# Optimization experiments

Hardware: AMD Instinct MI355X
Metric: run time of the kernel (lower is better)

Reference implementation:

```python
import jax, jax.numpy as jnp
import numpy as np
from jax.scipy.special import logsumexp

AND_SCALE = 1.0e5      # Minish scale used in And
EV_SCALE = 1.0e9       # Maxish scale / large_number used in Eventually
MASK_VALUE = -1.0e9    # -large_number fill for masked entries


def maxish(x, scale, axis):
    # stljax Maxish with scale > 0: logsumexp(scale*x)/scale (stable)
    return logsumexp(x * scale, axis=axis) / scale


def minish(x, scale, axis):
    return -maxish(-x, scale, axis)


def eventually_trace(s):
    # s: [B, T] robustness trace; interval = [0, T], padding='last'
    B, T = s.shape
    rows = jnp.arange(2 * T + 1)[:, None]   # padded time index i
    cols = jnp.arange(T)[None, :]           # output time index j
    # subsignal_mask (tril): j <= i ; time_interval_mask: (i - j <= T) & (j <= i)
    mask = (cols <= rows) & (rows - cols <= T)          # [2T+1, T]
    padded = jnp.concatenate(
        [s, jnp.broadcast_to(s[:, -1:], (B, T + 1))], axis=1
    )  # [B, 2T+1], padding='last'
    mat = jnp.where(mask[None, :, :], padded[:, :, None], MASK_VALUE)  # [B, 2T+1, T]
    return maxish(mat, EV_SCALE, axis=1)  # [B, T]


def channel_trace(c):
    # And(GreaterThan(c, 0), LessThan(c, 0)) -> Minish over stacked (c, -c)
    anded = minish(jnp.stack([c, -c], axis=-1), AND_SCALE, -1)  # [B, T]
    return eventually_trace(anded)


def setup_inputs() -> dict:
    key = jax.random.key(0)
    signal = jax.random.normal(key, (32, 1024, 2), dtype=jnp.float32)
    return {"signal": signal}


def reference(signal):
    x = signal[:, :, 0]
    y = signal[:, :, 1]
    final = channel_trace(x)
    final_2 = channel_trace(y)
    return (final, final_2)
```

## Files before the change

kernel.cpp:

```cpp
#include <hip/hip_runtime.h>
#include <cfloat>
#include <cmath>


__global__ __launch_bounds__(1024) void stl_suffix_kernel(
    const float* __restrict__ sig,
    float* __restrict__ out,
    int B, int T)
{
    const int b = blockIdx.x;
    const int t = threadIdx.x;

    __shared__ float sx[1024];
    __shared__ float sy[1024];

    float2 v = reinterpret_cast<const float2*>(sig)[b * T + t];

    const float AND_SCALE = 100000.0f;
    float ax = fabsf(v.x);
    float ay = fabsf(v.y);
    float vx = -ax - log1pf(expf(-2.0f * AND_SCALE * ax)) / AND_SCALE;
    float vy = -ay - log1pf(expf(-2.0f * AND_SCALE * ay)) / AND_SCALE;

    sx[t] = vx;
    sy[t] = vy;
    __syncthreads();

    #pragma unroll
    for (int st = 1; st < 1024; st <<= 1) {
        float ox = (t + st < 1024) ? sx[t + st] : -FLT_MAX;
        float oy = (t + st < 1024) ? sy[t + st] : -FLT_MAX;
        __syncthreads();
        sx[t] = fmaxf(sx[t], ox);
        sy[t] = fmaxf(sy[t], oy);
        __syncthreads();
    }

    out[b * T + t]          = sx[t];
    out[B * T + b * T + t]  = sy[t];
}

extern "C" void kernel_launch(void* const* d_in, const int* in_sizes, int n_in,
                              void* d_out, int out_size, void* d_ws, size_t ws_size,
                              hipStream_t stream) {
    const float* sig = (const float*)d_in[0];
    float* out = (float*)d_out;
    const int T = 1024;
    const int B = in_sizes[0] / (T * 2);
    stl_suffix_kernel<<<B, T, 0, stream>>>(sig, out, B, T);
}
```

Before: 9.881 us.

## Replace block-wide shared-memory suffix scan with single-wave register and shuffle scan

```diff
diff --git a/kernel.cpp b/kernel.cpp
--- a/kernel.cpp
+++ b/kernel.cpp
@@ -3,41 +3,56 @@
 #include <cmath>
 
 
-__global__ __launch_bounds__(1024) void stl_suffix_kernel(
+__global__ __launch_bounds__(64) void stl_suffix_wave(
     const float* __restrict__ sig,
     float* __restrict__ out,
     int B, int T)
 {
-    const int b = blockIdx.x;
-    const int t = threadIdx.x;
+    const int b    = blockIdx.x;
+    const int lane = threadIdx.x;
+    const int t0   = lane * 16;
 
-    __shared__ float sx[1024];
-    __shared__ float sy[1024];
-
-    float2 v = reinterpret_cast<const float2*>(sig)[b * T + t];
-
-    const float AND_SCALE = 100000.0f;
-    float ax = fabsf(v.x);
-    float ay = fabsf(v.y);
-    float vx = -ax - log1pf(expf(-2.0f * AND_SCALE * ax)) / AND_SCALE;
-    float vy = -ay - log1pf(expf(-2.0f * AND_SCALE * ay)) / AND_SCALE;
-
-    sx[t] = vx;
-    sy[t] = vy;
-    __syncthreads();
+    const float4* p = reinterpret_cast<const float4*>(sig) + (size_t)b * (T / 2) + lane * 8;
+    float vx[16], vy[16];
+    #pragma unroll
+    for (int i = 0; i < 8; ++i) {
+        float4 q = p[i];
+        vx[2 * i]     = fabsf(q.x);
+        vy[2 * i]     = fabsf(q.y);
+        vx[2 * i + 1] = fabsf(q.z);
+        vy[2 * i + 1] = fabsf(q.w);
+    }
 
     #pragma unroll
-    for (int st = 1; st < 1024; st <<= 1) {
-        float ox = (t + st < 1024) ? sx[t + st] : -FLT_MAX;
-        float oy = (t + st < 1024) ? sy[t + st] : -FLT_MAX;
-        __syncthreads();
-        sx[t] = fmaxf(sx[t], ox);
-        sy[t] = fmaxf(sy[t], oy);
-        __syncthreads();
+    for (int i = 14; i >= 0; --i) {
+        vx[i] = fminf(vx[i], vx[i + 1]);
+        vy[i] = fminf(vy[i], vy[i + 1]);
     }
 
-    out[b * T + t]          = sx[t];
-    out[B * T + b * T + t]  = sy[t];
+    float mx = vx[0], my = vy[0];
+    #pragma unroll
+    for (int off = 1; off < 64; off <<= 1) {
+        float ox = __shfl_down(mx, off);
+        float oy = __shfl_down(my, off);
+        if (lane + off < 64) { mx = fminf(mx, ox); my = fminf(my, oy); }
+    }
+    float ex = __shfl_down(mx, 1);
+    float ey = __shfl_down(my, 1);
+    if (lane == 63) { ex = FLT_MAX; ey = FLT_MAX; }
+
+    #pragma unroll
+    for (int i = 0; i < 16; ++i) {
+        vx[i] = -fminf(vx[i], ex);
+        vy[i] = -fminf(vy[i], ey);
+    }
+
+    float4* ox4 = reinterpret_cast<float4*>(out + (size_t)b * T + t0);
+    float4* oy4 = reinterpret_cast<float4*>(out + (size_t)B * T + (size_t)b * T + t0);
+    #pragma unroll
+    for (int i = 0; i < 4; ++i) {
+        ox4[i] = make_float4(vx[4 * i], vx[4 * i + 1], vx[4 * i + 2], vx[4 * i + 3]);
+        oy4[i] = make_float4(vy[4 * i], vy[4 * i + 1], vy[4 * i + 2], vy[4 * i + 3]);
+    }
 }
 
 extern "C" void kernel_launch(void* const* d_in, const int* in_sizes, int n_in,
@@ -47,5 +62,5 @@
     float* out = (float*)d_out;
     const int T = 1024;
     const int B = in_sizes[0] / (T * 2);
-    stl_suffix_kernel<<<B, T, 0, stream>>>(sig, out, B, T);
+    stl_suffix_wave<<<B, 64, 0, stream>>>(sig, out, B, T);
 }
```

After: 9.591 us. 2.9% less time.
